# Performance work log

Hardware: AMD Instinct MI355X
Metric: run time of the kernel (lower is better)

The kernel has to match this reference:

```python
import jax, jax.numpy as jnp
import numpy as np

N_COMP = 5
EPS = 0.1
BATCH = 2_097_152
BISECT_ITERS = 60
LAM_HI = 1e6  # upper bracket for the KL-constraint Lagrange multiplier


def setup_inputs() -> dict:
    key = jax.random.key(0)
    kx, kw, kb = jax.random.split(key, 3)
    # Positive inputs/weights keep q = x @ W.T + b > 0 (cp.kl_div domain).
    x = jax.random.uniform(kx, (BATCH, N_COMP), dtype=jnp.float32)
    W = jax.random.uniform(kw, (N_COMP, N_COMP), dtype=jnp.float32) * 0.5
    b = jax.random.uniform(kb, (N_COMP,), dtype=jnp.float32) * 0.5 + 0.1
    return {"x": x, "W": W, "b": b}


def _kl_ball_project(q, eps):
    """Solve min_p sum(kl_div(p,q)) s.t. sum(kl_div(p,r)) <= eps, sum(p)=1, p>=0
    with r = uniform (the module's first-call r_prev = ones/n, sum(r)=1).

    With sum(p)=1 the extra (-p + q) / (-p + r) terms of cp.kl_div are constants,
    so this is min KL(p||q) s.t. KL(p||r) <= eps on the simplex. KKT gives the
    closed-form geometric-mixture path p(lam) ~ q^{1/(1+lam)} * r^{lam/(1+lam)};
    we bisect on lam >= 0 to hit KL(p||r) = eps (lam=0 if already feasible).
    """
    n = q.shape[-1]
    logq = jnp.log(q)                                   # [B, n]
    log_r = -jnp.log(jnp.float32(n))                    # uniform r

    def p_of(lam, lq):
        t = (1.0 / (1.0 + lam))[..., None]              # [B, 1]
        return jax.nn.softmax(t * lq + (1.0 - t) * log_r, axis=-1)

    def g(lam, lq):  # constraint residual KL(p(lam) || r) - eps, shape [B]
        p = p_of(lam, lq)
        return jnp.sum(p * (jnp.log(p) - log_r), axis=-1) - eps

    # Bisection on a stop-gradient copy: lam is treated as a constant w.r.t. q
    # (envelope-style), so no solver iterations are stored for autodiff.
    lq_sg = jax.lax.stop_gradient(logq)
    zeros = jnp.zeros(q.shape[:-1], q.dtype)
    g0 = g(zeros, lq_sg)                                # feasibility at lam=0

    def body(carry, _):
        lo, hi = carry
        mid = 0.5 * (lo + hi)
        gm = g(mid, lq_sg)
        lo = jnp.where(gm > 0, mid, lo)
        hi = jnp.where(gm > 0, hi, mid)
        return (lo, hi), None

    (lo, hi), _ = jax.lax.scan(body, (zeros, jnp.full_like(zeros, LAM_HI)),
                               None, length=BISECT_ITERS)
    lam = jnp.where(g0 <= 0, 0.0, 0.5 * (lo + hi))      # exact 0 if feasible
    return p_of(lam, logq)


def reference(x, W, b):
    q = x @ W.T + b                                     # nn.Linear
    return _kl_ball_project(q, EPS)
```

## Files before the change

### kernel.cpp

```cpp
#include <hip/hip_runtime.h>
#include <math.h>

#define NC 5
#define EPS_F 0.1f

__global__ __launch_bounds__(256) void klproj_kernel(
    const float* __restrict__ x,
    const float* __restrict__ W,
    const float* __restrict__ b,
    float* __restrict__ out,
    int batch)
{
    int row = blockIdx.x * blockDim.x + threadIdx.x;
    if (row >= batch) return;

    float xv[NC];
#pragma unroll
    for (int k = 0; k < NC; ++k) xv[k] = x[row * NC + k];

    float s[NC];
    float m = -1e30f;
#pragma unroll
    for (int j = 0; j < NC; ++j) {
        float q = b[j];
#pragma unroll
        for (int k = 0; k < NC; ++k) q = fmaf(xv[k], W[j * NC + k], q);
        float sj = __logf(q);
        s[j] = sj;
        m = fmaxf(m, sj);
    }
    float u[NC];
#pragma unroll
    for (int j = 0; j < NC; ++j) u[j] = s[j] - m;

    const float logn = 1.6094379124341003f;

    auto eval = [&](float t, float& f, float& fp) {
        float Z = 0.f, T1 = 0.f, T2 = 0.f;
#pragma unroll
        for (int j = 0; j < NC; ++j) {
            float ej = __expf(t * u[j]);
            Z += ej;
            T1 = fmaf(ej, u[j], T1);
            T2 = fmaf(ej, u[j] * u[j], T2);
        }
        float rZ = 1.0f / Z;
        float Eu = T1 * rZ;
        float Eu2 = T2 * rZ;
        f  = fmaf(t, Eu, -__logf(Z)) + (logn - EPS_F);
        fp = t * (Eu2 - Eu * Eu);
    };

    float f1, fp1;
    eval(1.0f, f1, fp1);

    float t = 1.0f;
    if (f1 > 0.f) {
        float lo = 0.f, hi = 1.0f;
        float cand = 1.0f - f1 / fp1;
        t = (cand > lo && cand < hi) ? cand : 0.5f;
#pragma unroll
        for (int it = 0; it < 8; ++it) {
            float f, fp;
            eval(t, f, fp);
            if (f > 0.f) hi = t; else lo = t;
            float tn = t - f / fp;
            t = (tn > lo && tn < hi) ? tn : 0.5f * (lo + hi);
        }
    }

    float e[NC], Z = 0.f;
#pragma unroll
    for (int j = 0; j < NC; ++j) { e[j] = __expf(t * u[j]); Z += e[j]; }
    float rZ = 1.0f / Z;
#pragma unroll
    for (int j = 0; j < NC; ++j) out[row * NC + j] = e[j] * rZ;
}

extern "C" void kernel_launch(void* const* d_in, const int* in_sizes, int n_in,
                              void* d_out, int out_size, void* d_ws, size_t ws_size,
                              hipStream_t stream) {
    const float* x = (const float*)d_in[0];
    const float* W = (const float*)d_in[1];
    const float* b = (const float*)d_in[2];
    float* out = (float*)d_out;
    int batch = in_sizes[0] / NC;

    int block = 256;
    int grid = (batch + block - 1) / block;
    klproj_kernel<<<grid, block, 0, stream>>>(x, W, b, out, batch);
}
```

Before: 93.33 us.

## Switch root solve to Halley iterations and reuse final softmax evaluation

Replaces the safeguarded Newton solve for the temperature with a third-order Halley step that uses the third central moment. This allows cutting the loop from 8 to 4 evaluations. The exponentials from the last evaluation are reused for the output instead of being recomputed. Each evaluation now does more arithmetic (an extra moment accumulation), and the output comes from the last evaluated point rather than from a final Newton update. That could slightly lower accuracy if Halley has not converged.

```diff
diff --git a/kernel.cpp b/kernel.cpp
--- a/kernel.cpp
+++ b/kernel.cpp
@@ -18,7 +18,7 @@
 #pragma unroll
     for (int k = 0; k < NC; ++k) xv[k] = x[row * NC + k];
 
-    float s[NC];
+    float u[NC];
     float m = -1e30f;
 #pragma unroll
     for (int j = 0; j < NC; ++j) {
@@ -26,52 +26,63 @@
 #pragma unroll
         for (int k = 0; k < NC; ++k) q = fmaf(xv[k], W[j * NC + k], q);
         float sj = __logf(q);
-        s[j] = sj;
+        u[j] = sj;
         m = fmaxf(m, sj);
     }
-    float u[NC];
+    float u2[NC], u3[NC];
 #pragma unroll
-    for (int j = 0; j < NC; ++j) u[j] = s[j] - m;
+    for (int j = 0; j < NC; ++j) {
+        u[j] -= m;
+        u2[j] = u[j] * u[j];
+        u3[j] = u2[j] * u[j];
+    }
 
-    const float logn = 1.6094379124341003f;
+    const float logn_eps = 1.6094379124341003f - EPS_F;
 
-    auto eval = [&](float t, float& f, float& fp) {
-        float Z = 0.f, T1 = 0.f, T2 = 0.f;
+    float e[NC];
+    float Z, f, fp, fpp;
+    auto eval = [&](float t) {
+        float T1 = 0.f, T2 = 0.f, T3 = 0.f;
+        Z = 0.f;
 #pragma unroll
         for (int j = 0; j < NC; ++j) {
             float ej = __expf(t * u[j]);
+            e[j] = ej;
             Z += ej;
-            T1 = fmaf(ej, u[j], T1);
-            T2 = fmaf(ej, u[j] * u[j], T2);
+            T1 = fmaf(ej, u[j],  T1);
+            T2 = fmaf(ej, u2[j], T2);
+            T3 = fmaf(ej, u3[j], T3);
         }
-        float rZ = 1.0f / Z;
-        float Eu = T1 * rZ;
+        float rZ  = 1.0f / Z;
+        float Eu  = T1 * rZ;
         float Eu2 = T2 * rZ;
-        f  = fmaf(t, Eu, -__logf(Z)) + (logn - EPS_F);
-        fp = t * (Eu2 - Eu * Eu);
+        float Eu3 = T3 * rZ;
+        float var = fmaf(-Eu, Eu, Eu2);
+        float c   = fmaf(-2.0f * Eu, Eu, 3.0f * Eu2);
+        float mu3 = fmaf(-Eu, c, Eu3);
+        f   = fmaf(t, Eu, -__logf(Z)) + logn_eps;
+        fp  = t * var;
+        fpp = fmaf(t, mu3, var);
     };
 
-    float f1, fp1;
-    eval(1.0f, f1, fp1);
-
-    float t = 1.0f;
-    if (f1 > 0.f) {
+    eval(1.0f);
+    if (f > 0.f) {
         float lo = 0.f, hi = 1.0f;
-        float cand = 1.0f - f1 / fp1;
-        t = (cand > lo && cand < hi) ? cand : 0.5f;
+        float den  = fmaf(fp, fp, -0.5f * f * fpp);
+        float cand = 1.0f - f * fp / den;
+        float t = (cand > lo && cand < hi) ? cand : 0.5f;
 #pragma unroll
-        for (int it = 0; it < 8; ++it) {
-            float f, fp;
-            eval(t, f, fp);
+        for (int it = 0; it < 4; ++it) {
+            eval(t);
             if (f > 0.f) hi = t; else lo = t;
-            float tn = t - f / fp;
-            t = (tn > lo && tn < hi) ? tn : 0.5f * (lo + hi);
+            if (it < 3) {
+                den  = fmaf(fp, fp, -0.5f * f * fpp);
+                cand = t - f * fp / den;
+                t = (cand > lo && cand < hi) ? cand : 0.5f * (lo + hi);
+            }
         }
     }
 
-    float e[NC], Z = 0.f;
-#pragma unroll
-    for (int j = 0; j < NC; ++j) { e[j] = __expf(t * u[j]); Z += e[j]; }
     float rZ = 1.0f / Z;
 #pragma unroll
     for (int j = 0; j < NC; ++j) out[row * NC + j] = e[j] * rZ;
```

New measurement: 93.38 us. About the same (+0.1%).
